# Optimization experiments

Hardware: AMD Instinct MI355X
Metric: run time of the kernel (lower is better)

## Reference

```python
import jax, jax.numpy as jnp
import numpy as np

K = 9            # LCN box-filter size
EPS = 1e-6


def _box_sum(x):
    """9x9 box sum with zero padding 4, separable. x: [N,H,W] -> [N,H,W]."""
    xp = x[:, None]                                  # N,1,H,W
    kh = jnp.ones((1, 1, K, 1), x.dtype)
    kw = jnp.ones((1, 1, 1, K), x.dtype)
    y = jax.lax.conv_general_dilated(xp, kh, (1, 1), [(K // 2, K // 2), (0, 0)])
    y = jax.lax.conv_general_dilated(y, kw, (1, 1), [(0, 0), (K // 2, K // 2)])
    return y[:, 0]


def _lcn(img):
    """Faithful to torch: conv weight is ones(3,3,9,9)/81, i.e. the 'mean' SUMS over
    the 3 input channels of per-pixel 9x9 box means; every output channel is identical.
    So compute channel-sum once, box-filter it, and broadcast back over channels."""
    kk = float(K * K)
    mean_local = _box_sum(img.sum(axis=1)) / kk                 # N,H,W
    mean_sq_local = _box_sum((img * img).sum(axis=1)) / kk      # N,H,W
    std_local = (mean_sq_local - mean_local * mean_local) * kk / (kk - 1.0)
    m = mean_local[:, None]                                     # N,1,H,W (broadcasts over C)
    s = std_local[:, None]
    return (img - m) / (s + EPS), m, s


def _warp(right, disp):
    """Equivalent of affine_grid(identity) + grid -= (disp*2/W, 0) + grid_sample
    (bilinear, zeros padding, align_corners=False). Since the y-coordinate is the
    identity grid, iy == row index exactly, so sampling reduces to 1-D horizontal
    bilinear interpolation at source column ix = j - disp[n,i,j]."""
    N, C, H, W = right.shape
    ix = jnp.arange(W, dtype=right.dtype)[None, None, :] - disp   # N,H,W
    x0 = jnp.floor(ix)
    wx = ix - x0                                                  # frac weight for x1
    x0i = x0.astype(jnp.int32)
    x1i = x0i + 1
    v0 = ((x0i >= 0) & (x0i < W)).astype(right.dtype)             # zeros padding masks
    v1 = ((x1i >= 0) & (x1i < W)).astype(right.dtype)
    i0 = jnp.broadcast_to(jnp.clip(x0i, 0, W - 1)[:, None], right.shape)
    i1 = jnp.broadcast_to(jnp.clip(x1i, 0, W - 1)[:, None], right.shape)
    g0 = jnp.take_along_axis(right, i0, axis=3)                   # N,C,H,W
    g1 = jnp.take_along_axis(right, i1, axis=3)
    return g0 * (v0 * (1.0 - wx))[:, None] + g1 * (v1 * wx)[:, None]


def setup_inputs() -> dict:
    key = jax.random.key(0)
    k1, k2, k3 = jax.random.split(key, 3)
    N, C, H, W = 8, 3, 720, 1280
    left_img = jax.random.uniform(k1, (N, C, H, W), dtype=jnp.float32)
    right_img = jax.random.uniform(k2, (N, C, H, W), dtype=jnp.float32)
    dispmap = jax.random.uniform(k3, (N, H, W), dtype=jnp.float32) * 64.0  # pixels
    return {"left_img": left_img, "right_img": right_img, "dispmap": dispmap}


def reference(left_img, right_img, dispmap):
    recon_img = _warp(right_img, dispmap)
    recon_img_lcn, _, _ = _lcn(recon_img)
    left_img_lcn, _, left_std_local = _lcn(left_img)
    return jnp.abs((left_img_lcn - recon_img_lcn) * left_std_local).mean()
```

## Files before the change

### kernel.cpp

```cpp
#include <hip/hip_runtime.h>

#define NB 8
#define CC 3
#define HH 720
#define WW 1280
#define EPSL 1e-6f
#define HSEG 45
#define NSEG (HH / HSEG)
#define OUTC 56
#define NSTRIP 23
#define NITER (HSEG + 8)
#define NUNIT (NSTRIP * NSEG * NB)
#define NBLK (NUNIT / 4)

__global__ __launch_bounds__(256)
void fused_loss_kernel(const float* __restrict__ left,
                       const float* __restrict__ right,
                       const float* __restrict__ disp,
                       float* __restrict__ out)
{
    const int t    = threadIdx.x;
    const int lane = t & 63;
    const int u    = blockIdx.x * 4 + (t >> 6);
    const int strip = u % NSTRIP;
    const int hseg  = (u / NSTRIP) % NSEG;
    const int n     = u / (NSTRIP * NSEG);
    const int h0 = hseg * HSEG;
    const int gc  = strip * OUTC + lane - 4;
    const int gcc = min(max(gc, 0), WW - 1);
    const bool out_lane = (lane >= 4) && (lane < 4 + OUTC) && (gc < WW);
    const size_t plane = (size_t)HH * WW;
    const float* __restrict__ dispn  = disp  + (size_t)n * plane;
    const float* __restrict__ leftn  = left  + (size_t)n * CC * plane;
    const float* __restrict__ rightn = right + (size_t)n * CC * plane;

    float4 rg1 = make_float4(0.f,0.f,0.f,0.f);
    float4 rg2=rg1, rg3=rg1, rg4=rg1, rg5=rg1, rg6=rg1, rg7=rg1, rg8=rg1;
    float p1l0=0,p1l1=0,p1l2=0,p1r0=0,p1r1=0,p1r2=0;
    float p2l0=0,p2l1=0,p2l2=0,p2r0=0,p2r1=0,p2r2=0;
    float p3l0=0,p3l1=0,p3l2=0,p3r0=0,p3r1=0,p3r2=0;
    float p4l0=0,p4l1=0,p4l2=0,p4r0=0,p4r1=0,p4r2=0;

    const int r0 = h0 - 4;

    int rcl = min(max(r0, 0), HH - 1);
    size_t ro = (size_t)rcl * WW + gcc;
    float dA  = dispn[ro];
    float al0 = leftn[ro], al1 = leftn[plane + ro], al2 = leftn[2*plane + ro];
    rcl = min(max(r0 + 1, 0), HH - 1);
    ro  = (size_t)rcl * WW + gcc;
    float dB  = dispn[ro];
    float bl0 = leftn[ro], bl1 = leftn[plane + ro], bl2 = leftn[2*plane + ro];

    float aw0, aw1, ag00, ag01, ag10, ag11, ag20, ag21;
    {
        float ix  = (float)gc - dA;
        float x0f = floorf(ix), wx = ix - x0f;
        int x0i = (int)x0f, x1i = x0i + 1;
        float v0 = (x0i >= 0 && x0i < WW) ? 1.f : 0.f;
        float v1 = (x1i >= 0 && x1i < WW) ? 1.f : 0.f;
        int i0 = min(max(x0i, 0), WW - 1), i1 = min(max(x1i, 0), WW - 1);
        aw0 = v0 * (1.f - wx); aw1 = v1 * wx;
        size_t rb = (size_t)min(max(r0, 0), HH - 1) * WW;
        ag00 = rightn[rb + i0];           ag01 = rightn[rb + i1];
        ag10 = rightn[plane + rb + i0];   ag11 = rightn[plane + rb + i1];
        ag20 = rightn[2*plane + rb + i0]; ag21 = rightn[2*plane + rb + i1];
    }

    float4 vsum = make_float4(0.f,0.f,0.f,0.f);
    float acc = 0.f;

    for (int iter = 0; iter < NITER; ++iter) {
        const int r = r0 + iter;

        int rcl2 = min(max(r + 2, 0), HH - 1);
        size_t ro2 = (size_t)rcl2 * WW + gcc;
        float dC  = dispn[ro2];
        float cl0 = leftn[ro2], cl1 = leftn[plane + ro2], cl2 = leftn[2*plane + ro2];

        float bw0, bw1, bg00, bg01, bg10, bg11, bg20, bg21;
        {
            float ix  = (float)gc - dB;
            float x0f = floorf(ix), wx = ix - x0f;
            int x0i = (int)x0f, x1i = x0i + 1;
            float v0 = (x0i >= 0 && x0i < WW) ? 1.f : 0.f;
            float v1 = (x1i >= 0 && x1i < WW) ? 1.f : 0.f;
            int i0 = min(max(x0i, 0), WW - 1), i1 = min(max(x1i, 0), WW - 1);
            bw0 = v0 * (1.f - wx); bw1 = v1 * wx;
            size_t rb = (size_t)min(max(r + 1, 0), HH - 1) * WW;
            bg00 = rightn[rb + i0];           bg01 = rightn[rb + i1];
            bg10 = rightn[plane + rb + i0];   bg11 = rightn[plane + rb + i1];
            bg20 = rightn[2*plane + rb + i0]; bg21 = rightn[2*plane + rb + i1];
        }

        float rca = ag00*aw0 + ag01*aw1;
        float rcb = ag10*aw0 + ag11*aw1;
        float rcc = ag20*aw0 + ag21*aw1;
        bool valr = (r >= 0) && (r < HH) && (gc >= 0) && (gc < WW);
        float rx = al0 + al1 + al2;
        float ry = al0*al0 + al1*al1 + al2*al2;
        float rz = rca + rcb + rcc;
        float rw = rca*rca + rcb*rcb + rcc*rcc;
        rx = valr ? rx : 0.f;  ry = valr ? ry : 0.f;
        rz = valr ? rz : 0.f;  rw = valr ? rw : 0.f;

        const int sb = lane - 4;
        float hx = __shfl(rx, sb, 64);
        float hy = __shfl(ry, sb, 64);
        float hz = __shfl(rz, sb, 64);
        float hw = __shfl(rw, sb, 64);
#pragma unroll
        for (int k = 1; k < 9; ++k) {
            hx += __shfl(rx, sb + k, 64);
            hy += __shfl(ry, sb + k, 64);
            hz += __shfl(rz, sb + k, 64);
            hw += __shfl(rw, sb + k, 64);
        }

        vsum.x += hx; vsum.y += hy; vsum.z += hz; vsum.w += hw;

        if (iter >= 8) {
            float ml   = vsum.x * (1.f / 81.f);
            float msl  = vsum.y * (1.f / 81.f);
            float stdl = (msl - ml * ml) * (81.f / 80.f);
            float invl = 1.f / (stdl + EPSL);
            float mr   = vsum.z * (1.f / 81.f);
            float msr  = vsum.w * (1.f / 81.f);
            float stdr = (msr - mr * mr) * (81.f / 80.f);
            float invr = 1.f / (stdr + EPSL);
            if (out_lane) {
                float av, bv;
                av = (p4l0 - ml) * invl; bv = (p4r0 - mr) * invr;
                acc += fabsf((av - bv) * stdl);
                av = (p4l1 - ml) * invl; bv = (p4r1 - mr) * invr;
                acc += fabsf((av - bv) * stdl);
                av = (p4l2 - ml) * invl; bv = (p4r2 - mr) * invr;
                acc += fabsf((av - bv) * stdl);
            }
            vsum.x -= rg8.x; vsum.y -= rg8.y; vsum.z -= rg8.z; vsum.w -= rg8.w;
        }

        rg8 = rg7; rg7 = rg6; rg6 = rg5; rg5 = rg4; rg4 = rg3; rg3 = rg2; rg2 = rg1;
        rg1 = make_float4(hx, hy, hz, hw);
        p4l0=p3l0; p4l1=p3l1; p4l2=p3l2; p4r0=p3r0; p4r1=p3r1; p4r2=p3r2;
        p3l0=p2l0; p3l1=p2l1; p3l2=p2l2; p3r0=p2r0; p3r1=p2r1; p3r2=p2r2;
        p2l0=p1l0; p2l1=p1l1; p2l2=p1l2; p2r0=p1r0; p2r1=p1r1; p2r2=p1r2;
        p1l0=al0;  p1l1=al1;  p1l2=al2;  p1r0=rca;  p1r1=rcb;  p1r2=rcc;

        al0=bl0; al1=bl1; al2=bl2;
        aw0=bw0; aw1=bw1;
        ag00=bg00; ag01=bg01; ag10=bg10; ag11=bg11; ag20=bg20; ag21=bg21;
        dB=dC; bl0=cl0; bl1=cl1; bl2=cl2;
    }

#pragma unroll
    for (int off = 32; off > 0; off >>= 1)
        acc += __shfl_down(acc, off, 64);
    __shared__ float red[4];
    if (lane == 0) red[t >> 6] = acc;
    __syncthreads();
    if (t == 0) {
        float s = red[0] + red[1] + red[2] + red[3];
        const float inv_count = 1.f / ((float)NB * CC * HH * WW);
        atomicAdd(out, s * inv_count);
    }
}

extern "C" void kernel_launch(void* const* d_in, const int* in_sizes, int n_in,
                              void* d_out, int out_size, void* d_ws, size_t ws_size,
                              hipStream_t stream) {
    const float* left  = (const float*)d_in[0];
    const float* right = (const float*)d_in[1];
    const float* disp  = (const float*)d_in[2];
    float* out = (float*)d_out;

    hipMemsetAsync(out, 0, sizeof(float) * out_size, stream);

    hipLaunchKernelGGL(fused_loss_kernel, dim3(NBLK), dim3(256), 0, stream,
                       left, right, disp, out);
}
```

Before: 235.8 us.

## Use log-step shuffle box sum, unrolled ring buffers, fast reciprocal, shorter segments

Replaces the 9-tap shuffle sum with a prefix-doubling scheme (three doubling shuffles plus two more per quantity, down from nine). The row loop is unrolled by 8 so the row-history shift registers become statically indexed ring arrays, removing register moves. The IEEE divide is swapped for a hardware reciprocal plus one Newton step, and the row segment height drops from 45 to 40, giving more waves but more halo rows recomputed. Results can differ slightly in precision, and the overlapping shuffles wrap at wave edges, which must only touch non-output lanes.

```diff
diff --git a/kernel.cpp b/kernel.cpp
--- a/kernel.cpp
+++ b/kernel.cpp
@@ -5,13 +5,108 @@
 #define HH 720
 #define WW 1280
 #define EPSL 1e-6f
-#define HSEG 45
+#define HSEG 40
 #define NSEG (HH / HSEG)
 #define OUTC 56
 #define NSTRIP 23
-#define NITER (HSEG + 8)
-#define NUNIT (NSTRIP * NSEG * NB)
-#define NBLK (NUNIT / 4)
+#define NWAVES (NSTRIP * NSEG * NB)
+#define NBLK (NWAVES / 4)
+
+#define ITER_BODY(J, ITER, DO_OUT)                                         \
+  {                                                                        \
+    const int r = r0 + (ITER);                                             \
+                           \
+    int rcl2 = min(max(r + 2, 0), HH - 1);                                 \
+    size_t ro2 = (size_t)rcl2 * WW + gcc;                                  \
+    float dC  = dispn[ro2];                                                \
+    float cl0 = leftn[ro2];                                                \
+    float cl1 = leftn[plane + ro2];                                        \
+    float cl2 = leftn[2 * plane + ro2];                                    \
+                  \
+    float bw0, bw1, bg00, bg01, bg10, bg11, bg20, bg21;                    \
+    {                                                                      \
+      float ix  = (float)gc - dB;                                          \
+      float x0f = floorf(ix), wx = ix - x0f;                               \
+      int x0i = (int)x0f, x1i = x0i + 1;                                   \
+      float v0 = (x0i >= 0 && x0i < WW) ? 1.f : 0.f;                       \
+      float v1 = (x1i >= 0 && x1i < WW) ? 1.f : 0.f;                       \
+      int i0 = min(max(x0i, 0), WW - 1), i1 = min(max(x1i, 0), WW - 1);    \
+      bw0 = v0 * (1.f - wx); bw1 = v1 * wx;                                \
+      size_t rb = (size_t)min(max(r + 1, 0), HH - 1) * WW;                 \
+      bg00 = rightn[rb + i0];               bg01 = rightn[rb + i1];        \
+      bg10 = rightn[plane + rb + i0];       bg11 = rightn[plane + rb + i1];\
+      bg20 = rightn[2 * plane + rb + i0];   bg21 = rightn[2 * plane + rb + i1];\
+    }                                                                      \
+                               \
+    float rca = ag00 * aw0 + ag01 * aw1;                                   \
+    float rcb = ag10 * aw0 + ag11 * aw1;                                   \
+    float rcc = ag20 * aw0 + ag21 * aw1;                                   \
+    bool valr = (r >= 0) && (r < HH) && (gc >= 0) && (gc < WW);            \
+    float rx = al0 + al1 + al2;                                            \
+    float ry = al0 * al0 + al1 * al1 + al2 * al2;                          \
+    float rz = rca + rcb + rcc;                                            \
+    float rw = rca * rca + rcb * rcb + rcc * rcc;                          \
+    rx = valr ? rx : 0.f;  ry = valr ? ry : 0.f;                           \
+    rz = valr ? rz : 0.f;  rw = valr ? rw : 0.f;                           \
+               \
+    float hx, hy, hz, hw, s;                                               \
+    s = rx + __shfl(rx, lane + 1, 64);                                     \
+    s = s + __shfl(s, lane + 2, 64);                                       \
+    s = s + __shfl(s, lane + 4, 64);                                       \
+    hx = __shfl(s, lane - 4, 64) + __shfl(rx, lane + 4, 64);               \
+    s = ry + __shfl(ry, lane + 1, 64);                                     \
+    s = s + __shfl(s, lane + 2, 64);                                       \
+    s = s + __shfl(s, lane + 4, 64);                                       \
+    hy = __shfl(s, lane - 4, 64) + __shfl(ry, lane + 4, 64);               \
+    s = rz + __shfl(rz, lane + 1, 64);                                     \
+    s = s + __shfl(s, lane + 2, 64);                                       \
+    s = s + __shfl(s, lane + 4, 64);                                       \
+    hz = __shfl(s, lane - 4, 64) + __shfl(rz, lane + 4, 64);               \
+    s = rw + __shfl(rw, lane + 1, 64);                                     \
+    s = s + __shfl(s, lane + 2, 64);                                       \
+    s = s + __shfl(s, lane + 4, 64);                                       \
+    hw = __shfl(s, lane - 4, 64) + __shfl(rw, lane + 4, 64);               \
+                                             \
+    vsum.x += hx; vsum.y += hy; vsum.z += hz; vsum.w += hw;                \
+    if (DO_OUT) {                                                          \
+      float ml   = vsum.x * (1.f / 81.f);                                  \
+      float msl  = vsum.y * (1.f / 81.f);                                  \
+      float stdl = (msl - ml * ml) * (81.f / 80.f);                        \
+      float denl = stdl + EPSL;                                            \
+      float invl = __builtin_amdgcn_rcpf(denl);                            \
+      invl = fmaf(fmaf(-denl, invl, 1.f), invl, invl);                     \
+      float mr   = vsum.z * (1.f / 81.f);                                  \
+      float msr  = vsum.w * (1.f / 81.f);                                  \
+      float stdr = (msr - mr * mr) * (81.f / 80.f);                        \
+      float denr = stdr + EPSL;                                            \
+      float invr = __builtin_amdgcn_rcpf(denr);                            \
+      invr = fmaf(fmaf(-denr, invr, 1.f), invr, invr);                     \
+      if (out_lane) {                                                      \
+        float av, bv;                                                      \
+        av = (pxl0[(J) & 3] - ml) * invl;                                  \
+        bv = (pxr0[(J) & 3] - mr) * invr;                                  \
+        acc += fabsf((av - bv) * stdl);                                    \
+        av = (pxl1[(J) & 3] - ml) * invl;                                  \
+        bv = (pxr1[(J) & 3] - mr) * invr;                                  \
+        acc += fabsf((av - bv) * stdl);                                    \
+        av = (pxl2[(J) & 3] - ml) * invl;                                  \
+        bv = (pxr2[(J) & 3] - mr) * invr;                                  \
+        acc += fabsf((av - bv) * stdl);                                    \
+      }                                                                    \
+      float4 oldr = ring[(J) & 7];            \
+      vsum.x -= oldr.x; vsum.y -= oldr.y;                                  \
+      vsum.z -= oldr.z; vsum.w -= oldr.w;                                  \
+    }                                                                      \
+    ring[(J) & 7] = make_float4(hx, hy, hz, hw);                           \
+    pxl0[(J) & 3] = al0; pxl1[(J) & 3] = al1; pxl2[(J) & 3] = al2;         \
+    pxr0[(J) & 3] = rca; pxr1[(J) & 3] = rcb; pxr2[(J) & 3] = rcc;         \
+    \
+    al0 = bl0; al1 = bl1; al2 = bl2;                                       \
+    aw0 = bw0; aw1 = bw1;                                                  \
+    ag00 = bg00; ag01 = bg01; ag10 = bg10; ag11 = bg11;                    \
+    ag20 = bg20; ag21 = bg21;                                              \
+    dB = dC; bl0 = cl0; bl1 = cl1; bl2 = cl2;                              \
+  }
 
 __global__ __launch_bounds__(256)
 void fused_loss_kernel(const float* __restrict__ left,
@@ -33,24 +128,20 @@
     const float* __restrict__ dispn  = disp  + (size_t)n * plane;
     const float* __restrict__ leftn  = left  + (size_t)n * CC * plane;
     const float* __restrict__ rightn = right + (size_t)n * CC * plane;
+    const int r0 = h0 - 4;
 
-    float4 rg1 = make_float4(0.f,0.f,0.f,0.f);
-    float4 rg2=rg1, rg3=rg1, rg4=rg1, rg5=rg1, rg6=rg1, rg7=rg1, rg8=rg1;
-    float p1l0=0,p1l1=0,p1l2=0,p1r0=0,p1r1=0,p1r2=0;
-    float p2l0=0,p2l1=0,p2l2=0,p2r0=0,p2r1=0,p2r2=0;
-    float p3l0=0,p3l1=0,p3l2=0,p3r0=0,p3r1=0,p3r2=0;
-    float p4l0=0,p4l1=0,p4l2=0,p4r0=0,p4r1=0,p4r2=0;
-
-    const int r0 = h0 - 4;
+    float4 ring[8];
+    float pxl0[4], pxl1[4], pxl2[4];
+    float pxr0[4], pxr1[4], pxr2[4];
 
     int rcl = min(max(r0, 0), HH - 1);
     size_t ro = (size_t)rcl * WW + gcc;
     float dA  = dispn[ro];
-    float al0 = leftn[ro], al1 = leftn[plane + ro], al2 = leftn[2*plane + ro];
+    float al0 = leftn[ro], al1 = leftn[plane + ro], al2 = leftn[2 * plane + ro];
     rcl = min(max(r0 + 1, 0), HH - 1);
     ro  = (size_t)rcl * WW + gcc;
     float dB  = dispn[ro];
-    float bl0 = leftn[ro], bl1 = leftn[plane + ro], bl2 = leftn[2*plane + ro];
+    float bl0 = leftn[ro], bl1 = leftn[plane + ro], bl2 = leftn[2 * plane + ro];
 
     float aw0, aw1, ag00, ag01, ag10, ag11, ag20, ag21;
     {
@@ -62,95 +153,21 @@
         int i0 = min(max(x0i, 0), WW - 1), i1 = min(max(x1i, 0), WW - 1);
         aw0 = v0 * (1.f - wx); aw1 = v1 * wx;
         size_t rb = (size_t)min(max(r0, 0), HH - 1) * WW;
-        ag00 = rightn[rb + i0];           ag01 = rightn[rb + i1];
-        ag10 = rightn[plane + rb + i0];   ag11 = rightn[plane + rb + i1];
-        ag20 = rightn[2*plane + rb + i0]; ag21 = rightn[2*plane + rb + i1];
+        ag00 = rightn[rb + i0];             ag01 = rightn[rb + i1];
+        ag10 = rightn[plane + rb + i0];     ag11 = rightn[plane + rb + i1];
+        ag20 = rightn[2 * plane + rb + i0]; ag21 = rightn[2 * plane + rb + i1];
     }
 
-    float4 vsum = make_float4(0.f,0.f,0.f,0.f);
+    float4 vsum = make_float4(0.f, 0.f, 0.f, 0.f);
     float acc = 0.f;
 
-    for (int iter = 0; iter < NITER; ++iter) {
-        const int r = r0 + iter;
+#pragma unroll
+    for (int j = 0; j < 8; ++j) ITER_BODY(j, j, false)
 
-        int rcl2 = min(max(r + 2, 0), HH - 1);
-        size_t ro2 = (size_t)rcl2 * WW + gcc;
-        float dC  = dispn[ro2];
-        float cl0 = leftn[ro2], cl1 = leftn[plane + ro2], cl2 = leftn[2*plane + ro2];
-
-        float bw0, bw1, bg00, bg01, bg10, bg11, bg20, bg21;
-        {
-            float ix  = (float)gc - dB;
-            float x0f = floorf(ix), wx = ix - x0f;
-            int x0i = (int)x0f, x1i = x0i + 1;
-            float v0 = (x0i >= 0 && x0i < WW) ? 1.f : 0.f;
-            float v1 = (x1i >= 0 && x1i < WW) ? 1.f : 0.f;
-            int i0 = min(max(x0i, 0), WW - 1), i1 = min(max(x1i, 0), WW - 1);
-            bw0 = v0 * (1.f - wx); bw1 = v1 * wx;
-            size_t rb = (size_t)min(max(r + 1, 0), HH - 1) * WW;
-            bg00 = rightn[rb + i0];           bg01 = rightn[rb + i1];
-            bg10 = rightn[plane + rb + i0];   bg11 = rightn[plane + rb + i1];
-            bg20 = rightn[2*plane + rb + i0]; bg21 = rightn[2*plane + rb + i1];
-        }
-
-        float rca = ag00*aw0 + ag01*aw1;
-        float rcb = ag10*aw0 + ag11*aw1;
-        float rcc = ag20*aw0 + ag21*aw1;
-        bool valr = (r >= 0) && (r < HH) && (gc >= 0) && (gc < WW);
-        float rx = al0 + al1 + al2;
-        float ry = al0*al0 + al1*al1 + al2*al2;
-        float rz = rca + rcb + rcc;
-        float rw = rca*rca + rcb*rcb + rcc*rcc;
-        rx = valr ? rx : 0.f;  ry = valr ? ry : 0.f;
-        rz = valr ? rz : 0.f;  rw = valr ? rw : 0.f;
-
-        const int sb = lane - 4;
-        float hx = __shfl(rx, sb, 64);
-        float hy = __shfl(ry, sb, 64);
-        float hz = __shfl(rz, sb, 64);
-        float hw = __shfl(rw, sb, 64);
+    for (int big = 1; big < 6; ++big) {
+        const int base = big * 8;
 #pragma unroll
-        for (int k = 1; k < 9; ++k) {
-            hx += __shfl(rx, sb + k, 64);
-            hy += __shfl(ry, sb + k, 64);
-            hz += __shfl(rz, sb + k, 64);
-            hw += __shfl(rw, sb + k, 64);
-        }
-
-        vsum.x += hx; vsum.y += hy; vsum.z += hz; vsum.w += hw;
-
-        if (iter >= 8) {
-            float ml   = vsum.x * (1.f / 81.f);
-            float msl  = vsum.y * (1.f / 81.f);
-            float stdl = (msl - ml * ml) * (81.f / 80.f);
-            float invl = 1.f / (stdl + EPSL);
-            float mr   = vsum.z * (1.f / 81.f);
-            float msr  = vsum.w * (1.f / 81.f);
-            float stdr = (msr - mr * mr) * (81.f / 80.f);
-            float invr = 1.f / (stdr + EPSL);
-            if (out_lane) {
-                float av, bv;
-                av = (p4l0 - ml) * invl; bv = (p4r0 - mr) * invr;
-                acc += fabsf((av - bv) * stdl);
-                av = (p4l1 - ml) * invl; bv = (p4r1 - mr) * invr;
-                acc += fabsf((av - bv) * stdl);
-                av = (p4l2 - ml) * invl; bv = (p4r2 - mr) * invr;
-                acc += fabsf((av - bv) * stdl);
-            }
-            vsum.x -= rg8.x; vsum.y -= rg8.y; vsum.z -= rg8.z; vsum.w -= rg8.w;
-        }
-
-        rg8 = rg7; rg7 = rg6; rg6 = rg5; rg5 = rg4; rg4 = rg3; rg3 = rg2; rg2 = rg1;
-        rg1 = make_float4(hx, hy, hz, hw);
-        p4l0=p3l0; p4l1=p3l1; p4l2=p3l2; p4r0=p3r0; p4r1=p3r1; p4r2=p3r2;
-        p3l0=p2l0; p3l1=p2l1; p3l2=p2l2; p3r0=p2r0; p3r1=p2r1; p3r2=p2r2;
-        p2l0=p1l0; p2l1=p1l1; p2l2=p1l2; p2r0=p1r0; p2r1=p1r1; p2r2=p1r2;
-        p1l0=al0;  p1l1=al1;  p1l2=al2;  p1r0=rca;  p1r1=rcb;  p1r2=rcc;
-
-        al0=bl0; al1=bl1; al2=bl2;
-        aw0=bw0; aw1=bw1;
-        ag00=bg00; ag01=bg01; ag10=bg10; ag11=bg11; ag20=bg20; ag21=bg21;
-        dB=dC; bl0=cl0; bl1=cl1; bl2=cl2;
+        for (int j = 0; j < 8; ++j) ITER_BODY(j, base + j, true)
     }
 
 #pragma unroll
@@ -160,9 +177,9 @@
     if (lane == 0) red[t >> 6] = acc;
     __syncthreads();
     if (t == 0) {
-        float s = red[0] + red[1] + red[2] + red[3];
+        float sred = red[0] + red[1] + red[2] + red[3];
         const float inv_count = 1.f / ((float)NB * CC * HH * WW);
-        atomicAdd(out, s * inv_count);
+        atomicAdd(out, sred * inv_count);
     }
 }
 
```

New measurement: 245.1 us. +3.9%, slower.
